# Performance work log

Hardware: AMD Instinct MI355X
Metric: run time of the kernel (lower is better)

The kernel has to match this reference:

```python
import jax, jax.numpy as jnp
import numpy as np

N_NODES = 50000
IN_C, HID_C, OUT_C = 128, 128, 64
N_EDGES = 600000
DROPOUT_P = 0.5


def setup_inputs() -> dict:
    key = jax.random.key(0)
    k1, k2, k3, k4, k5, k6 = jax.random.split(key, 6)
    x = jax.random.normal(k1, (N_NODES, IN_C), dtype=jnp.float32)
    edge_index = jax.random.randint(k2, (2, N_EDGES), 0, N_NODES, dtype=jnp.int64)
    s1 = 1.0 / np.sqrt(IN_C)
    s2 = 1.0 / np.sqrt(HID_C)
    W1 = jax.random.uniform(k3, (IN_C, HID_C), jnp.float32, -s1, s1)
    b1 = jnp.zeros((HID_C,), jnp.float32)
    W2 = jax.random.uniform(k4, (HID_C, OUT_C), jnp.float32, -s2, s2)
    b2 = jnp.zeros((OUT_C,), jnp.float32)
    return {"x": x, "W1": W1, "b1": b1, "W2": W2, "b2": b2, "edge_index": edge_index}


def reference(x, W1, b1, W2, b2, edge_index):
    N = x.shape[0]
    self_loops = jnp.arange(N, dtype=edge_index.dtype)
    src = jnp.concatenate([edge_index[0], self_loops])  # [E+N]
    dst = jnp.concatenate([edge_index[1], self_loops])
    # symmetric GCN normalization with self-loops (gcn_norm)
    deg = jax.ops.segment_sum(jnp.ones(dst.shape, x.dtype), dst, num_segments=N)
    dinv = jnp.where(deg > 0, jax.lax.rsqrt(deg), 0.0)
    norm = dinv[src] * dinv[dst]  # [E+N]

    def conv(h, W, b):
        h = h @ W  # dense transform first (smaller message dim)
        msg = h[src] * norm[:, None]  # gather + scale, [E+N, C]
        return jax.ops.segment_sum(msg, dst, num_segments=N) + b

    h = jax.nn.relu(conv(x, W1, b1))
    # dropout p=0.5 with fixed key (training mode, deterministic reference)
    keep = jax.random.bernoulli(jax.random.key(42), 1.0 - DROPOUT_P, h.shape)
    h = jnp.where(keep, h / (1.0 - DROPOUT_P), 0.0)
    return conv(h, W2, b2)
```

## Files before the change

### kernel.cpp

```cpp
#include <hip/hip_runtime.h>


#define NN      50000
#define INC     128
#define HIDC    128
#define OUTC    64
#define NE      600000
#define NB      ((NN + 255) / 256)
#define CAP     64

typedef unsigned short bf16_t;
typedef short bf16x8 __attribute__((ext_vector_type(8)));
typedef float f32x4  __attribute__((ext_vector_type(4)));

__device__ __forceinline__ unsigned short f2bf(float f) {
  unsigned u = __float_as_uint(f);
  u += 0x7fffu + ((u >> 16) & 1u);
  return (unsigned short)(u >> 16);
}

__device__ __forceinline__ float dinv_of(int c) {
  return 1.0f / sqrtf((float)(c + 1));
}

__device__ __forceinline__ void tf_round(unsigned &x0, unsigned &x1, int r) {
  x0 += x1;
  x1 = (x1 << r) | (x1 >> (32 - r));
  x1 ^= x0;
}

__device__ __forceinline__ void threefry_0_42(unsigned &x0, unsigned &x1) {
  const unsigned ks0 = 0u, ks1 = 42u, ks2 = 0x1BD11BDAu ^ 42u;
  x0 += ks0; x1 += ks1;
  tf_round(x0,x1,13); tf_round(x0,x1,15); tf_round(x0,x1,26); tf_round(x0,x1, 6);
  x0 += ks1; x1 += ks2 + 1u;
  tf_round(x0,x1,17); tf_round(x0,x1,29); tf_round(x0,x1,16); tf_round(x0,x1,24);
  x0 += ks2; x1 += ks0 + 2u;
  tf_round(x0,x1,13); tf_round(x0,x1,15); tf_round(x0,x1,26); tf_round(x0,x1, 6);
  x0 += ks0; x1 += ks1 + 3u;
  tf_round(x0,x1,17); tf_round(x0,x1,29); tf_round(x0,x1,16); tf_round(x0,x1,24);
  x0 += ks1; x1 += ks2 + 4u;
  tf_round(x0,x1,13); tf_round(x0,x1,15); tf_round(x0,x1,26); tf_round(x0,x1, 6);
  x0 += ks2; x1 += ks0 + 5u;
}

__device__ __forceinline__ bool keep_bit(unsigned idx) {
  unsigned x0 = 0u, x1 = idx;
  threefry_0_42(x0, x1);
  return ((x0 ^ x1) & 0x80000000u) == 0u;
}

__global__ __launch_bounds__(256)
void prep0(const unsigned* __restrict__ ew, int* __restrict__ flag,
           int* __restrict__ cnt) {
  const int b = blockIdx.x, t = threadIdx.x;
  if (b < NB) {
    int idx = b * 256 + t;
    if (idx < NN) cnt[idx] = 0;
  } else {
    __shared__ unsigned acc[256];
    unsigned v = 0;
    for (int i = t; i < 2048; i += 256) v |= ew[2 * i + 1];
    acc[t] = v;
    __syncthreads();
    for (int s = 128; s > 0; s >>= 1) {
      if (t < s) acc[t] |= acc[t + s];
      __syncthreads();
    }
    if (t == 0) *flag = (acc[0] == 0u) ? 1 : 0;
  }
}

__global__ __launch_bounds__(256)
void bucket_direct(const void* __restrict__ ei, const int* __restrict__ flag,
                   int* __restrict__ cnt, int* __restrict__ ssrc) {
  int t = blockIdx.x * 256 + threadIdx.x;
  if (t >= NE) return;
  int s, d;
  if (*flag) {
    s = (int)((const long long*)ei)[t];
    d = (int)((const long long*)ei)[NE + t];
  } else {
    s = ((const int*)ei)[t];
    d = ((const int*)ei)[NE + t];
  }
  int slot = atomicAdd(&cnt[d], 1);
  if (slot < CAP) ssrc[d * CAP + slot] = s;
}

template<int C, bool IN_BF16>
__global__ __launch_bounds__(256, 3)
void gemm_mfma(const void* __restrict__ Xv, const float* __restrict__ W,
               const int* __restrict__ cnt, bf16_t* __restrict__ Ab, int n) {
  constexpr int K  = 128;
  constexpr int KS = 136;
  constexpr int CT16 = C / 16;
  __shared__ bf16_t xs[64 * KS];
  __shared__ bf16_t wsT[C * KS];

  const int tid = threadIdx.x;
  const int rb  = blockIdx.x * 64;

  for (int i = tid; i < C * (K / 8); i += 256) {
    int nn = i % C, kc = i / C;
    ushort4 lo, hi;
    lo.x = f2bf(W[(size_t)(kc * 8 + 0) * C + nn]);
    lo.y = f2bf(W[(size_t)(kc * 8 + 1) * C + nn]);
    lo.z = f2bf(W[(size_t)(kc * 8 + 2) * C + nn]);
    lo.w = f2bf(W[(size_t)(kc * 8 + 3) * C + nn]);
    hi.x = f2bf(W[(size_t)(kc * 8 + 4) * C + nn]);
    hi.y = f2bf(W[(size_t)(kc * 8 + 5) * C + nn]);
    hi.z = f2bf(W[(size_t)(kc * 8 + 6) * C + nn]);
    hi.w = f2bf(W[(size_t)(kc * 8 + 7) * C + nn]);
    *(ushort4*)&wsT[nn * KS + kc * 8]     = lo;
    *(ushort4*)&wsT[nn * KS + kc * 8 + 4] = hi;
  }
  for (int i = tid; i < 64 * (K / 4); i += 256) {
    int r = i >> 5, kq = i & 31;
    int row = rb + r;
    ushort4 o = make_ushort4(0, 0, 0, 0);
    if (row < n) {
      if (IN_BF16) {
        o = *(const ushort4*)((const bf16_t*)Xv + (size_t)row * K + kq * 4);
      } else {
        float4 v = *(const float4*)((const float*)Xv + (size_t)row * K + kq * 4);
        o.x = f2bf(v.x); o.y = f2bf(v.y); o.z = f2bf(v.z); o.w = f2bf(v.w);
      }
    }
    *(ushort4*)&xs[r * KS + kq * 4] = o;
  }
  __syncthreads();

  const int wv   = tid >> 6;
  const int lane = tid & 63;
  const int m    = lane & 15;
  const int q    = lane >> 4;

  f32x4 acc[CT16];
#pragma unroll
  for (int c = 0; c < CT16; c++) acc[c] = (f32x4){0.f, 0.f, 0.f, 0.f};

#pragma unroll
  for (int k0 = 0; k0 < K; k0 += 32) {
    bf16x8 a = *(bf16x8*)&xs[(wv * 16 + m) * KS + k0 + q * 8];
#pragma unroll
    for (int c = 0; c < CT16; c++) {
      bf16x8 b = *(bf16x8*)&wsT[(c * 16 + m) * KS + k0 + q * 8];
      acc[c] = __builtin_amdgcn_mfma_f32_16x16x32_bf16(a, b, acc[c], 0, 0, 0);
    }
  }

  const int rowq = rb + wv * 16 + q * 4;
#pragma unroll
  for (int r = 0; r < 4; r++) {
    int row = rowq + r;
    if (row < n) {
      float dv = dinv_of(cnt[row]);
#pragma unroll
      for (int c = 0; c < CT16; c++)
        Ab[(size_t)row * C + c * 16 + m] = f2bf(acc[c][r] * dv);
    }
  }
}

__device__ __forceinline__ void acc_u2(float4 &a, uint2 v) {
  a.x += __uint_as_float(v.x << 16);
  a.y += __uint_as_float(v.x & 0xffff0000u);
  a.z += __uint_as_float(v.y << 16);
  a.w += __uint_as_float(v.y & 0xffff0000u);
}

__global__ __launch_bounds__(256)
void agg1(const bf16_t* __restrict__ A1b, const int* __restrict__ cnt,
          const int* __restrict__ ssrc, const float* __restrict__ b1,
          bf16_t* __restrict__ Hb) {
  int node = (blockIdx.x * 256 + threadIdx.x) >> 5;
  int lane = threadIdx.x & 31;
  if (node >= NN) return;

  const uint2* A4 = (const uint2*)A1b;
  const int cn = cnt[node];
  const float dn = dinv_of(cn);
  float4 acc = make_float4(0.f, 0.f, 0.f, 0.f);
  acc_u2(acc, A4[(size_t)node * 32 + lane]);
  int e = node * CAP;
  int end = e + min(cn, CAP);
  for (; e + 3 < end; e += 4) {
    int s0 = ssrc[e], s1 = ssrc[e+1], s2 = ssrc[e+2], s3 = ssrc[e+3];
    uint2 v0 = A4[(size_t)s0 * 32 + lane];
    uint2 v1 = A4[(size_t)s1 * 32 + lane];
    uint2 v2 = A4[(size_t)s2 * 32 + lane];
    uint2 v3 = A4[(size_t)s3 * 32 + lane];
    acc_u2(acc, v0); acc_u2(acc, v1); acc_u2(acc, v2); acc_u2(acc, v3);
  }
  for (; e < end; e++)
    acc_u2(acc, A4[(size_t)ssrc[e] * 32 + lane]);

  int col = lane * 4;
  float4 bb = *(const float4*)&b1[col];
  float h0 = fmaxf(acc.x * dn + bb.x, 0.f);
  float h1 = fmaxf(acc.y * dn + bb.y, 0.f);
  float h2 = fmaxf(acc.z * dn + bb.z, 0.f);
  float h3 = fmaxf(acc.w * dn + bb.w, 0.f);
  unsigned base = (unsigned)node * HIDC + (unsigned)col;
  ushort4 o;
  o.x = keep_bit(base)     ? f2bf(2.f * h0) : 0;
  o.y = keep_bit(base + 1) ? f2bf(2.f * h1) : 0;
  o.z = keep_bit(base + 2) ? f2bf(2.f * h2) : 0;
  o.w = keep_bit(base + 3) ? f2bf(2.f * h3) : 0;
  ((ushort4*)Hb)[(size_t)node * 32 + lane] = o;
}

__global__ __launch_bounds__(256)
void agg2(const bf16_t* __restrict__ A2b, const int* __restrict__ cnt,
          const int* __restrict__ ssrc, const float* __restrict__ b2,
          float* __restrict__ out) {
  int node = (blockIdx.x * 256 + threadIdx.x) >> 4;
  int lane = threadIdx.x & 15;
  if (node >= NN) return;

  const uint2* A4 = (const uint2*)A2b;
  const int cn = cnt[node];
  const float dn = dinv_of(cn);
  float4 acc = make_float4(0.f, 0.f, 0.f, 0.f);
  acc_u2(acc, A4[(size_t)node * 16 + lane]);
  int e = node * CAP;
  int end = e + min(cn, CAP);
  for (; e + 3 < end; e += 4) {
    int s0 = ssrc[e], s1 = ssrc[e+1], s2 = ssrc[e+2], s3 = ssrc[e+3];
    uint2 v0 = A4[(size_t)s0 * 16 + lane];
    uint2 v1 = A4[(size_t)s1 * 16 + lane];
    uint2 v2 = A4[(size_t)s2 * 16 + lane];
    uint2 v3 = A4[(size_t)s3 * 16 + lane];
    acc_u2(acc, v0); acc_u2(acc, v1); acc_u2(acc, v2); acc_u2(acc, v3);
  }
  for (; e < end; e++)
    acc_u2(acc, A4[(size_t)ssrc[e] * 16 + lane]);

  float4 bb = *(const float4*)&b2[lane * 4];
  ((float4*)out)[(size_t)node * 16 + lane] =
    make_float4(acc.x*dn + bb.x, acc.y*dn + bb.y, acc.z*dn + bb.z, acc.w*dn + bb.w);
}

extern "C" void kernel_launch(void* const* d_in, const int* in_sizes, int n_in,
                              void* d_out, int out_size, void* d_ws, size_t ws_size,
                              hipStream_t stream) {
  const float* x  = (const float*)d_in[0];
  const float* W1 = (const float*)d_in[1];
  const float* b1 = (const float*)d_in[2];
  const float* W2 = (const float*)d_in[3];
  const float* b2 = (const float*)d_in[4];
  const void*  ei = d_in[5];
  float* out = (float*)d_out;

  int*    flag = (int*)d_ws;
  int*    cnt  = flag + 64;
  int*    ssrc = cnt + 50048;
  bf16_t* A1b  = (bf16_t*)(ssrc + NN * CAP);
  bf16_t* Hb   = A1b + 6400000;
  bf16_t* A2b  = Hb + 6400000;

  prep0<<<NB + 1, 256, 0, stream>>>((const unsigned*)ei, flag, cnt);

  bucket_direct<<<(NE + 255) / 256, 256, 0, stream>>>(ei, flag, cnt, ssrc);

  const int rtiles = (NN + 63) / 64;

  gemm_mfma<HIDC, false><<<rtiles, 256, 0, stream>>>(x, W1, cnt, A1b, NN);
  agg1<<<(NN * 32 + 255) / 256, 256, 0, stream>>>(A1b, cnt, ssrc, b1, Hb);

  gemm_mfma<OUTC, true><<<rtiles, 256, 0, stream>>>(Hb, W2, cnt, A2b, NN);
  agg2<<<(NN * 16 + 255) / 256, 256, 0, stream>>>(A2b, cnt, ssrc, b2, out);
}
```

Baseline: 194.5 us.

## Fuse edge bucketing into first GEMM and move source normalization into aggregation

The separate bucketing kernel is folded into the first MFMA GEMM: each of the 782 blocks reads 768 edges, does the degree atomics, and writes the bucketed sources alongside its tile loads. The first GEMM then cannot know final degrees, so it no longer scales rows by dinv. agg1 instead applies the source dinv per edge by reading cnt[s] and using rsqrt. This removes one kernel launch and overlaps atomic traffic with GEMM staging, at the cost of an extra scattered cnt read per edge in agg1.

```diff
diff --git a/kernel.cpp b/kernel.cpp
--- a/kernel.cpp
+++ b/kernel.cpp
@@ -71,27 +71,12 @@
   }
 }
 
-__global__ __launch_bounds__(256)
-void bucket_direct(const void* __restrict__ ei, const int* __restrict__ flag,
-                   int* __restrict__ cnt, int* __restrict__ ssrc) {
-  int t = blockIdx.x * 256 + threadIdx.x;
-  if (t >= NE) return;
-  int s, d;
-  if (*flag) {
-    s = (int)((const long long*)ei)[t];
-    d = (int)((const long long*)ei)[NE + t];
-  } else {
-    s = ((const int*)ei)[t];
-    d = ((const int*)ei)[NE + t];
-  }
-  int slot = atomicAdd(&cnt[d], 1);
-  if (slot < CAP) ssrc[d * CAP + slot] = s;
-}
-
-template<int C, bool IN_BF16>
 __global__ __launch_bounds__(256, 3)
-void gemm_mfma(const void* __restrict__ Xv, const float* __restrict__ W,
-               const int* __restrict__ cnt, bf16_t* __restrict__ Ab, int n) {
+void gemm1_bucket(const float* __restrict__ X, const float* __restrict__ W,
+                  const void* __restrict__ ei, const int* __restrict__ flag,
+                  int* __restrict__ cnt, int* __restrict__ ssrc,
+                  bf16_t* __restrict__ Ab) {
+  constexpr int C  = HIDC;
   constexpr int K  = 128;
   constexpr int KS = 136;
   constexpr int CT16 = C / 16;
@@ -100,6 +85,30 @@
 
   const int tid = threadIdx.x;
   const int rb  = blockIdx.x * 64;
+
+  const int eb = blockIdx.x * 768;
+  int es[3], ed[3];
+  bool ev[3];
+  const bool i64 = (*flag != 0);
+#pragma unroll
+  for (int j = 0; j < 3; j++) {
+    int e = eb + j * 256 + tid;
+    ev[j] = (e < NE);
+    es[j] = 0; ed[j] = 0;
+    if (ev[j]) {
+      if (i64) {
+        es[j] = (int)((const long long*)ei)[e];
+        ed[j] = (int)((const long long*)ei)[NE + e];
+      } else {
+        es[j] = ((const int*)ei)[e];
+        ed[j] = ((const int*)ei)[NE + e];
+      }
+    }
+  }
+  int slot[3];
+#pragma unroll
+  for (int j = 0; j < 3; j++)
+    slot[j] = ev[j] ? atomicAdd(&cnt[ed[j]], 1) : CAP;
 
   for (int i = tid; i < C * (K / 8); i += 256) {
     int nn = i % C, kc = i / C;
@@ -119,6 +128,81 @@
     int r = i >> 5, kq = i & 31;
     int row = rb + r;
     ushort4 o = make_ushort4(0, 0, 0, 0);
+    if (row < NN) {
+      float4 v = *(const float4*)(X + (size_t)row * K + kq * 4);
+      o.x = f2bf(v.x); o.y = f2bf(v.y); o.z = f2bf(v.z); o.w = f2bf(v.w);
+    }
+    *(ushort4*)&xs[r * KS + kq * 4] = o;
+  }
+
+#pragma unroll
+  for (int j = 0; j < 3; j++)
+    if (ev[j] && slot[j] < CAP) ssrc[ed[j] * CAP + slot[j]] = es[j];
+
+  __syncthreads();
+
+  const int wv   = tid >> 6;
+  const int lane = tid & 63;
+  const int m    = lane & 15;
+  const int q    = lane >> 4;
+
+  f32x4 acc[CT16];
+#pragma unroll
+  for (int c = 0; c < CT16; c++) acc[c] = (f32x4){0.f, 0.f, 0.f, 0.f};
+
+#pragma unroll
+  for (int k0 = 0; k0 < K; k0 += 32) {
+    bf16x8 a = *(bf16x8*)&xs[(wv * 16 + m) * KS + k0 + q * 8];
+#pragma unroll
+    for (int c = 0; c < CT16; c++) {
+      bf16x8 b = *(bf16x8*)&wsT[(c * 16 + m) * KS + k0 + q * 8];
+      acc[c] = __builtin_amdgcn_mfma_f32_16x16x32_bf16(a, b, acc[c], 0, 0, 0);
+    }
+  }
+
+  const int rowq = rb + wv * 16 + q * 4;
+#pragma unroll
+  for (int r = 0; r < 4; r++) {
+    int row = rowq + r;
+    if (row < NN) {
+#pragma unroll
+      for (int c = 0; c < CT16; c++)
+        Ab[(size_t)row * C + c * 16 + m] = f2bf(acc[c][r]);
+    }
+  }
+}
+
+template<int C, bool IN_BF16>
+__global__ __launch_bounds__(256, 3)
+void gemm_mfma(const void* __restrict__ Xv, const float* __restrict__ W,
+               const int* __restrict__ cnt, bf16_t* __restrict__ Ab, int n) {
+  constexpr int K  = 128;
+  constexpr int KS = 136;
+  constexpr int CT16 = C / 16;
+  __shared__ bf16_t xs[64 * KS];
+  __shared__ bf16_t wsT[C * KS];
+
+  const int tid = threadIdx.x;
+  const int rb  = blockIdx.x * 64;
+
+  for (int i = tid; i < C * (K / 8); i += 256) {
+    int nn = i % C, kc = i / C;
+    ushort4 lo, hi;
+    lo.x = f2bf(W[(size_t)(kc * 8 + 0) * C + nn]);
+    lo.y = f2bf(W[(size_t)(kc * 8 + 1) * C + nn]);
+    lo.z = f2bf(W[(size_t)(kc * 8 + 2) * C + nn]);
+    lo.w = f2bf(W[(size_t)(kc * 8 + 3) * C + nn]);
+    hi.x = f2bf(W[(size_t)(kc * 8 + 4) * C + nn]);
+    hi.y = f2bf(W[(size_t)(kc * 8 + 5) * C + nn]);
+    hi.z = f2bf(W[(size_t)(kc * 8 + 6) * C + nn]);
+    hi.w = f2bf(W[(size_t)(kc * 8 + 7) * C + nn]);
+    *(ushort4*)&wsT[nn * KS + kc * 8]     = lo;
+    *(ushort4*)&wsT[nn * KS + kc * 8 + 4] = hi;
+  }
+  for (int i = tid; i < 64 * (K / 4); i += 256) {
+    int r = i >> 5, kq = i & 31;
+    int row = rb + r;
+    ushort4 o = make_ushort4(0, 0, 0, 0);
     if (row < n) {
       if (IN_BF16) {
         o = *(const ushort4*)((const bf16_t*)Xv + (size_t)row * K + kq * 4);
@@ -170,6 +254,17 @@
   a.w += __uint_as_float(v.y & 0xffff0000u);
 }
 
+__device__ __forceinline__ void acc_u2s(float4 &a, uint2 v, float dv) {
+  a.x = fmaf(dv, __uint_as_float(v.x << 16),         a.x);
+  a.y = fmaf(dv, __uint_as_float(v.x & 0xffff0000u), a.y);
+  a.z = fmaf(dv, __uint_as_float(v.y << 16),         a.z);
+  a.w = fmaf(dv, __uint_as_float(v.y & 0xffff0000u), a.w);
+}
+
+__device__ __forceinline__ float dinv_fast(int c) {
+  return rsqrtf((float)(c + 1));
+}
+
 __global__ __launch_bounds__(256)
 void agg1(const bf16_t* __restrict__ A1b, const int* __restrict__ cnt,
           const int* __restrict__ ssrc, const float* __restrict__ b1,
@@ -182,7 +277,7 @@
   const int cn = cnt[node];
   const float dn = dinv_of(cn);
   float4 acc = make_float4(0.f, 0.f, 0.f, 0.f);
-  acc_u2(acc, A4[(size_t)node * 32 + lane]);
+  acc_u2s(acc, A4[(size_t)node * 32 + lane], dn);
   int e = node * CAP;
   int end = e + min(cn, CAP);
   for (; e + 3 < end; e += 4) {
@@ -191,10 +286,17 @@
     uint2 v1 = A4[(size_t)s1 * 32 + lane];
     uint2 v2 = A4[(size_t)s2 * 32 + lane];
     uint2 v3 = A4[(size_t)s3 * 32 + lane];
-    acc_u2(acc, v0); acc_u2(acc, v1); acc_u2(acc, v2); acc_u2(acc, v3);
-  }
-  for (; e < end; e++)
-    acc_u2(acc, A4[(size_t)ssrc[e] * 32 + lane]);
+    float q0 = dinv_fast(cnt[s0]);
+    float q1 = dinv_fast(cnt[s1]);
+    float q2 = dinv_fast(cnt[s2]);
+    float q3 = dinv_fast(cnt[s3]);
+    acc_u2s(acc, v0, q0); acc_u2s(acc, v1, q1);
+    acc_u2s(acc, v2, q2); acc_u2s(acc, v3, q3);
+  }
+  for (; e < end; e++) {
+    int s = ssrc[e];
+    acc_u2s(acc, A4[(size_t)s * 32 + lane], dinv_fast(cnt[s]));
+  }
 
   int col = lane * 4;
   float4 bb = *(const float4*)&b1[col];
@@ -262,11 +364,9 @@
 
   prep0<<<NB + 1, 256, 0, stream>>>((const unsigned*)ei, flag, cnt);
 
-  bucket_direct<<<(NE + 255) / 256, 256, 0, stream>>>(ei, flag, cnt, ssrc);
-
   const int rtiles = (NN + 63) / 64;
 
-  gemm_mfma<HIDC, false><<<rtiles, 256, 0, stream>>>(x, W1, cnt, A1b, NN);
+  gemm1_bucket<<<rtiles, 256, 0, stream>>>(x, W1, ei, flag, cnt, ssrc, A1b);
   agg1<<<(NN * 32 + 255) / 256, 256, 0, stream>>>(A1b, cnt, ssrc, b1, Hb);
 
   gemm_mfma<OUTC, true><<<rtiles, 256, 0, stream>>>(Hb, W2, cnt, A2b, NN);
```

After: 185.9 us. 1.05x faster.
